# Kernel optimization log

Hardware: AMD Instinct MI355X
Metric: run time of the kernel (lower is better)

The kernel has to match this reference:

```python
import jax, jax.numpy as jnp
import numpy as np

DIM = 128
B, H, W = 2, 256, 256


def conv2d(x, w, b, groups=1):
    # x: [B,C,H,W], w: [O, C//groups, kh, kw] (OIHW)
    y = jax.lax.conv_general_dilated(
        x, w, window_strides=(1, 1), padding='SAME',
        dimension_numbers=('NCHW', 'OIHW', 'NCHW'),
        feature_group_count=groups)
    return y + b[None, :, None, None]


def l2_normalize(x, axis=-1, eps=1e-12):
    # matches torch.nn.functional.normalize (p=2)
    n = jnp.sqrt(jnp.sum(x * x, axis=axis, keepdims=True))
    return x / jnp.maximum(n, eps)


def setup_inputs() -> dict:
    key = jax.random.key(0)
    ks = jax.random.split(key, 14)
    d = DIM
    h = d // 2
    s = 0.05
    return {
        'x': jax.random.normal(ks[0], (B, d, H, W), dtype=jnp.float32),
        'w_qkv': jax.random.normal(ks[1], (3 * d, d, 1, 1), dtype=jnp.float32) * s,
        'b_qkv': jax.random.normal(ks[2], (3 * d,), dtype=jnp.float32) * s,
        'w_q': jax.random.normal(ks[3], (d, 1, 3, 3), dtype=jnp.float32) * s,
        'b_q': jax.random.normal(ks[4], (d,), dtype=jnp.float32) * s,
        'w_k': jax.random.normal(ks[5], (d, 1, 3, 3), dtype=jnp.float32) * s,
        'b_k': jax.random.normal(ks[6], (d,), dtype=jnp.float32) * s,
        'w_v1': jax.random.normal(ks[7], (h, 2, 3, 3), dtype=jnp.float32) * s,  # groups=d/2, 2 in-ch per group
        'b_v1': jax.random.normal(ks[8], (h,), dtype=jnp.float32) * s,
        'w_v2': jax.random.normal(ks[9], (h, 1, 3, 3), dtype=jnp.float32) * s,  # depthwise on d/2
        'b_v2': jax.random.normal(ks[10], (h,), dtype=jnp.float32) * s,
        'temperature': jnp.ones((d, 1, 1), dtype=jnp.float32),
        'w_po': jax.random.normal(ks[11], (d, d, 1, 1), dtype=jnp.float32) * s,
        'b_po': jax.random.normal(ks[12], (d,), dtype=jnp.float32) * s,
    }


def reference(x, w_qkv, b_qkv, w_q, b_q, w_k, b_k, w_v1, b_v1, w_v2, b_v2,
              temperature, w_po, b_po):
    d = x.shape[1]
    h = d // 2
    # 1x1 conv -> qkv, then split
    qkv = conv2d(x, w_qkv, b_qkv)                     # [B,3d,H,W]
    q, k, v = jnp.split(qkv, 3, axis=1)
    # depthwise 3x3 on q, k
    q = conv2d(q, w_q, b_q, groups=d)
    k = conv2d(k, w_k, b_k, groups=d)
    # MDC on v: grouped conv (2->1 per group), depthwise, concat, sigmoid gate
    x1 = conv2d(v, w_v1, b_v1, groups=h)              # [B,d/2,H,W]
    x2 = conv2d(x1, w_v2, b_v2, groups=h)             # [B,d/2,H,W]
    v = jax.nn.sigmoid(v) * jnp.concatenate([x1, x2], axis=1)
    # per-channel row attention: normalize over W, [B,C,H,H] scores
    q1 = l2_normalize(q, axis=-1)
    k1 = l2_normalize(k, axis=-1)
    scores = jnp.einsum('bchw,bcgw->bchg', q1, k1) * temperature[None]  # [B,C,H,H]
    attn = jax.nn.softmax(scores, axis=-1)
    out = jnp.einsum('bchg,bcgw->bchw', attn, v)      # [B,C,H,W]
    return conv2d(out, w_po, b_po)
```

## Files before the change

kernel.cpp:

```cpp
#include <hip/hip_runtime.h>

typedef unsigned short u16;
typedef unsigned int u32;

#define HW 256
#define PIX 65536

#define WS_T1   100663296ull
#define WS_K1   134217728ull
#define WS_VP   167772160ull
#define WS_NEED 201326592ull

typedef __attribute__((ext_vector_type(8))) short s8v;
typedef __attribute__((ext_vector_type(4))) float f4v;

__device__ __forceinline__ float bu2f(u16 u){ union{u32 i; float f;} x; x.i=((u32)u)<<16; return x.f; }
__device__ __forceinline__ u16 f2bu(float f){ union{float f; u32 i;} x; x.f=f; u32 i=x.i; return (u16)((i + 0x7FFFu + ((i>>16)&1u))>>16); }
__device__ __forceinline__ float sigm(float x){ return 1.0f/(1.0f+__expf(-x)); }
__device__ __forceinline__ u16 cvt_el(float v){ return f2bu(v); }
__device__ __forceinline__ u16 cvt_el(u16 v){ return v; }
__device__ __forceinline__ int swz(int r, int c){ return r*256 + (((c>>3) ^ (r&7))<<3) + (c&7); }
__device__ __forceinline__ int pswz(int p, int c){ return (p<<7) + (((c>>3) ^ (p&7))<<3) + (c&7); }
__device__ __forceinline__ int vt_el(int w, int gb){
  int q = (w & 15) ^ gb ^ ((w >> 4) & 7);
  return ((w >> 4) << 10) + (gb << 7) + (q << 3);
}

template<int OC, typename TIN, bool F32>
__global__ __launch_bounds__(256,1) void k_gemmP(const TIN* __restrict__ in, const float* __restrict__ Wg,
                                                 const float* __restrict__ bias, int O_total,
                                                 void* __restrict__ outv){
  extern __shared__ u16 lds[];
  u16* Wl = lds;
  u16* Xl = lds + OC*128;
  int t = threadIdx.x;
  for (int i = t; i < OC*128; i += 256){
    int o = i >> 7, c = i & 127;
    Wl[(o << 7) | (c ^ ((o & 7) << 3))] = f2bu(Wg[(size_t)o*128 + c]);
  }
  int p_blk = blockIdx.x * 256;
  int b = p_blk >> 16;
  int p0 = p_blk & 65535;
  {
    const TIN* col = in + (size_t)b*128*PIX + p0 + t;
    #pragma unroll 8
    for (int c2 = 0; c2 < 64; ++c2){
      int c = c2 * 2;
      u16 v0 = cvt_el(col[(size_t)c*PIX]);
      u16 v1 = cvt_el(col[(size_t)(c+1)*PIX]);
      *(u32*)(Xl + pswz(t, c)) = (u32)v0 | ((u32)v1 << 16);
    }
  }
  __syncthreads();

  int wv = t >> 6, l = t & 63;
  int lg = l >> 4, lr = l & 15;
  int p_in0 = p0 + wv*16 + lr;

  s8v bf[4][4];
  #pragma unroll
  for (int pt = 0; pt < 4; ++pt){
    int p = wv*16 + pt*64 + lr;
    #pragma unroll
    for (int ks = 0; ks < 4; ++ks)
      bf[pt][ks] = *(const s8v*)(Xl + pswz(p, ks*32 + lg*8));
  }

  for (int ot = 0; ot < OC / 16; ++ot){
    f4v acc[4];
    #pragma unroll
    for (int pt = 0; pt < 4; ++pt) acc[pt] = (f4v){0.f,0.f,0.f,0.f};
    int o = (ot << 4) + lr;
    const u16* wl = Wl + (o << 7);
    int sw = (o & 7) << 3;
    #pragma unroll
    for (int ks = 0; ks < 4; ++ks){
      s8v a = *(const s8v*)(wl + ((((ks << 5) + (lg << 3)) ^ sw)));
      #pragma unroll
      for (int pt = 0; pt < 4; ++pt)
        acc[pt] = __builtin_amdgcn_mfma_f32_16x16x32_bf16(a, bf[pt][ks], acc[pt], 0, 0, 0);
    }
    #pragma unroll
    for (int j = 0; j < 4; ++j){
      int o_row = (ot << 4) + (lg << 2) + j;
      float bv = bias[o_row];
      size_t base = ((size_t)(b * O_total + o_row)) << 16;
      #pragma unroll
      for (int pt = 0; pt < 4; ++pt){
        if (F32){
          ((float*)outv)[base + p_in0 + pt*64] = acc[pt][j] + bv;
        } else {
          ((u16*)outv)[base + p_in0 + pt*64] = f2bu(acc[pt][j] + bv);
        }
      }
    }
  }
}
#define GP384_LDS ((384*128 + 256*128) * 2)
#define GP128_LDS ((128*128 + 256*128) * 2)

__global__ __launch_bounds__(256) void k_dwqk2(const u16* __restrict__ qkv,
                                               const float* __restrict__ w_q, const float* __restrict__ b_q,
                                               const float* __restrict__ w_k, const float* __restrict__ b_k,
                                               u16* __restrict__ q1, u16* __restrict__ k1){
  __shared__ u16 ins[18*272];
  int t = threadIdx.x;
  int chunk = blockIdx.x;
  int c = blockIdx.y;
  int which = blockIdx.z & 1, b = blockIdx.z >> 1;
  const u16* in = qkv + ((size_t)(b*384 + which*128 + c)) * PIX;

  #pragma unroll
  for (int i = t; i < 612; i += 256) ((uint4*)ins)[i] = make_uint4(0,0,0,0);
  __syncthreads();
  int r0 = chunk*16 - 1;
  for (int i = t; i < 576; i += 256){
    int j = i >> 5, k = i & 31;
    int r = r0 + j;
    if (r >= 0 && r < HW)
      *(uint4*)(ins + j*272 + 8 + k*8) = *(const uint4*)(in + r*HW + k*8);
  }
  __syncthreads();

  const float* wk = (which ? w_k : w_q) + c*9;
  float K0=wk[0],K1=wk[1],K2=wk[2],K3=wk[3],K4=wk[4],K5=wk[5],K6=wk[6],K7=wk[7],K8=wk[8];
  float bias = (which ? b_k : b_q)[c];

  int wv = t >> 6, l = t & 63;
  int cb = l * 4;
  float wr[3][6];
  auto ldrow = [&](int j, int slot){
    ushort4 m = *(const ushort4*)(ins + j*272 + 8 + cb);
    wr[slot][0] = bu2f(ins[j*272 + 7 + cb]);
    wr[slot][1] = bu2f(m.x); wr[slot][2] = bu2f(m.y);
    wr[slot][3] = bu2f(m.z); wr[slot][4] = bu2f(m.w);
    wr[slot][5] = bu2f(ins[j*272 + 12 + cb]);
  };
  int rb = wv * 4;
  ldrow(rb, 0); ldrow(rb+1, 1);
  u16* outp = (which ? k1 : q1) + ((size_t)(b*128 + c)) * PIX;
  #pragma unroll
  for (int s = 0; s < 4; ++s){
    ldrow(rb + s + 2, (s+2)%3);
    const float* T = wr[s%3];
    const float* M = wr[(s+1)%3];
    const float* Bo = wr[(s+2)%3];
    float o[4]; float ss = 0.f;
    #pragma unroll
    for (int d = 0; d < 4; ++d){
      float a = bias;
      a = fmaf(K0, T[d], a);  a = fmaf(K1, T[d+1], a);  a = fmaf(K2, T[d+2], a);
      a = fmaf(K3, M[d], a);  a = fmaf(K4, M[d+1], a);  a = fmaf(K5, M[d+2], a);
      a = fmaf(K6, Bo[d], a); a = fmaf(K7, Bo[d+1], a); a = fmaf(K8, Bo[d+2], a);
      o[d] = a;
      ss = fmaf(a, a, ss);
    }
    #pragma unroll
    for (int m = 1; m < 64; m <<= 1) ss += __shfl_xor(ss, m, 64);
    float sc = 1.0f / fmaxf(sqrtf(ss), 1e-12f);
    int row = chunk*16 + rb + s;
    ushort4 pk;
    pk.x = f2bu(o[0]*sc); pk.y = f2bu(o[1]*sc); pk.z = f2bu(o[2]*sc); pk.w = f2bu(o[3]*sc);
    *(ushort4*)(outp + row*HW + cb) = pk;
  }
}

#define MDC_LDS (2*36*272*2 + 34*272*4)

__global__ __launch_bounds__(256,1) void k_mdc2(const u16* __restrict__ qkv,
                                                const float* __restrict__ w_v1, const float* __restrict__ b_v1,
                                                const float* __restrict__ w_v2, const float* __restrict__ b_v2,
                                                u16* __restrict__ vp){
  extern __shared__ char sm[];
  u16*   ins = (u16*)sm;
  float* x1s = (float*)(sm + 2*36*272*2);
  int t = threadIdx.x;
  int chunk = blockIdx.x;
  int g = blockIdx.y;
  int b = blockIdx.z;
  const u16* vbase = qkv + ((size_t)(b*384 + 256)) * PIX;

  #pragma unroll
  for (int i = t; i < 2*36*34; i += 256) ((uint4*)ins)[i] = make_uint4(0,0,0,0);
  for (int i = t; i < 34*68; i += 256) ((uint4*)x1s)[i] = make_uint4(0,0,0,0);
  __syncthreads();
  int r0 = chunk*32 - 2;
  #pragma unroll
  for (int ch = 0; ch < 2; ++ch){
    const u16* src = vbase + (size_t)(2*g + ch) * PIX;
    for (int i = t; i < 1152; i += 256){
      int j = i >> 5, k = i & 31;
      int r = r0 + j;
      if (r >= 0 && r < HW)
        *(uint4*)(ins + ch*36*272 + j*272 + 8 + k*8) = *(const uint4*)(src + r*HW + k*8);
    }
  }
  __syncthreads();

  float W1[18];
  #pragma unroll
  for (int i = 0; i < 18; ++i) W1[i] = w_v1[g*18 + i];
  float B1 = b_v1[g];
  int cb = t + 8;
  float win[2][3][3];
  #pragma unroll
  for (int ch = 0; ch < 2; ++ch)
    #pragma unroll
    for (int rr = 0; rr < 2; ++rr)
      #pragma unroll
      for (int k = 0; k < 3; ++k)
        win[ch][rr][k] = bu2f(ins[ch*36*272 + rr*272 + cb - 1 + k]);
  #pragma unroll
  for (int j = 0; j < 34; ++j){
    #pragma unroll
    for (int ch = 0; ch < 2; ++ch)
      #pragma unroll
      for (int k = 0; k < 3; ++k)
        win[ch][(j+2)%3][k] = bu2f(ins[ch*36*272 + (j+2)*272 + cb - 1 + k]);
    float v = B1;
    #pragma unroll
    for (int ch = 0; ch < 2; ++ch)
      #pragma unroll
      for (int i = 0; i < 3; ++i)
        #pragma unroll
        for (int k = 0; k < 3; ++k)
          v = fmaf(W1[ch*9 + i*3 + k], win[ch][(j+i)%3][k], v);
    int gr = chunk*32 - 1 + j;
    if (gr >= 0 && gr < HW) x1s[j*272 + cb] = v;
  }
  __syncthreads();

  float W2[9];
  #pragma unroll
  for (int i = 0; i < 9; ++i) W2[i] = w_v2[g*9 + i];
  float B2 = b_v2[g];
  const u16* vg   = vbase + (size_t)g * PIX;
  const u16* vg64 = vbase + (size_t)(64 + g) * PIX;
  u16* out0 = vp + ((size_t)(b*128 + g)) * PIX;
  u16* out1 = vp + ((size_t)(b*128 + 64 + g)) * PIX;
  float xw[3][3];
  #pragma unroll
  for (int rr = 0; rr < 2; ++rr)
    #pragma unroll
    for (int k = 0; k < 3; ++k)
      xw[rr][k] = x1s[rr*272 + cb - 1 + k];
  #pragma unroll
  for (int h = 0; h < 32; ++h){
    #pragma unroll
    for (int k = 0; k < 3; ++k)
      xw[(h+2)%3][k] = x1s[(h+2)*272 + cb - 1 + k];
    float x2 = B2;
    #pragma unroll
    for (int i = 0; i < 3; ++i)
      #pragma unroll
      for (int k = 0; k < 3; ++k)
        x2 = fmaf(W2[i*3 + k], xw[(h+i)%3][k], x2);
    int gr = chunk*32 + h;
    float g1 = sigm(bu2f(vg[gr*HW + t]));
    float g2 = sigm(bu2f(vg64[gr*HW + t]));
    float x1c = xw[(h+1)%3][1];
    out0[gr*HW + t] = f2bu(g1 * x1c);
    out1[gr*HW + t] = f2bu(g2 * x2);
  }
}

#define AT2_LDS 163840

__global__ __launch_bounds__(512,1) void k_attn2(const u16* __restrict__ q1, const u16* __restrict__ k1,
                                                 const u16* __restrict__ vp, const float* __restrict__ temp,
                                                 u16* __restrict__ out){
  extern __shared__ char smemraw[];
  u16* Qs = (u16*)smemraw;
  u16* Ks = Qs + 32768;
  u16* Ps = Ks + 16384;
  const int t = threadIdx.x;
  const int l = t & 63;
  const int wv = t >> 6;
  const int c15 = l & 15, h = l >> 4;
  const int blk = blockIdx.x;
  const int plane = blk >> 1, hf = blk & 1;
  const u16* qp  = q1 + (size_t)plane * PIX + hf*128*HW;
  const u16* kp  = k1 + (size_t)plane * PIX;
  const u16* vpp = vp + (size_t)plane * PIX;
  u16* op = out + (size_t)plane * PIX + hf*128*HW;
  const float tc = temp[plane & 127];

  #pragma unroll
  for (int i = 0; i < 8; ++i){
    int c = t + i*512; int row = c >> 5, bc = (c & 31) << 3;
    *(uint4*)(Qs + swz(row, bc)) = *(const uint4*)(qp + row*HW + bc);
  }
  #pragma unroll
  for (int i = 0; i < 4; ++i){
    int c = t + i*512; int row = c >> 5, bc = (c & 31) << 3;
    *(uint4*)(Ks + swz(row, bc)) = *(const uint4*)(kp + row*HW + bc);
  }
  __syncthreads();

  const int r_a = wv*16 + c15;
  s8v qa[8];
  #pragma unroll
  for (int ks = 0; ks < 8; ++ks)
    qa[ks] = *(const s8v*)(Qs + swz(r_a, ks*32 + h*8));

  f4v sacc[16];
  #pragma unroll
  for (int i = 0; i < 16; ++i) sacc[i] = (f4v){0.f,0.f,0.f,0.f};

  uint4 pf[4];
  #pragma unroll
  for (int gt = 0; gt < 4; ++gt){
    {
      const u16* src = (gt < 3) ? (kp + (gt+1)*64*HW) : vpp;
      #pragma unroll
      for (int i = 0; i < 4; ++i){
        int c = t + i*512; int row = c >> 5, bc = (c & 31) << 3;
        pf[i] = *(const uint4*)(src + row*HW + bc);
      }
    }
    #pragma unroll
    for (int gi = 0; gi < 4; ++gi){
      f4v acc = sacc[gt*4 + gi];
      #pragma unroll
      for (int ks = 0; ks < 8; ++ks){
        s8v b = *(const s8v*)(Ks + swz(gi*16 + c15, ks*32 + h*8));
        acc = __builtin_amdgcn_mfma_f32_16x16x32_bf16(qa[ks], b, acc, 0, 0, 0);
      }
      sacc[gt*4 + gi] = acc;
    }
    __syncthreads();
    #pragma unroll
    for (int i = 0; i < 4; ++i){
      int c = t + i*512; int row = c >> 5, bc = (c & 31) << 3;
      *(uint4*)(Ks + swz(row, bc)) = pf[i];
    }
    __syncthreads();
  }

  float mj[4] = {-1e30f,-1e30f,-1e30f,-1e30f};
  #pragma unroll
  for (int i = 0; i < 16; ++i)
    #pragma unroll
    for (int j = 0; j < 4; ++j){
      sacc[i][j] *= tc;
      mj[j] = fmaxf(mj[j], sacc[i][j]);
    }
  #pragma unroll
  for (int j = 0; j < 4; ++j){
    mj[j] = fmaxf(mj[j], __shfl_xor(mj[j], 1, 64));
    mj[j] = fmaxf(mj[j], __shfl_xor(mj[j], 2, 64));
    mj[j] = fmaxf(mj[j], __shfl_xor(mj[j], 4, 64));
    mj[j] = fmaxf(mj[j], __shfl_xor(mj[j], 8, 64));
  }
  float sj[4] = {0.f,0.f,0.f,0.f};
  #pragma unroll
  for (int i = 0; i < 16; ++i)
    #pragma unroll
    for (int j = 0; j < 4; ++j){
      float e = __expf(sacc[i][j] - mj[j]);
      sacc[i][j] = e;
      sj[j] += e;
    }
  #pragma unroll
  for (int j = 0; j < 4; ++j){
    sj[j] += __shfl_xor(sj[j], 1, 64);
    sj[j] += __shfl_xor(sj[j], 2, 64);
    sj[j] += __shfl_xor(sj[j], 4, 64);
    sj[j] += __shfl_xor(sj[j], 8, 64);
    sj[j] = 1.0f / sj[j];
  }
  #pragma unroll
  for (int i = 0; i < 16; ++i)
    #pragma unroll
    for (int j = 0; j < 4; ++j)
      Ps[swz(wv*16 + h*4 + j, i*16 + c15)] = f2bu(sacc[i][j] * sj[j]);
  __syncthreads();

  f4v oacc[16];
  #pragma unroll
  for (int i = 0; i < 16; ++i) oacc[i] = (f4v){0.f,0.f,0.f,0.f};

  #pragma unroll
  for (int gt = 0; gt < 4; ++gt){
    if (gt < 3){
      #pragma unroll
      for (int i = 0; i < 4; ++i){
        int c = t + i*512; int row = c >> 5, bc = (c & 31) << 3;
        pf[i] = *(const uint4*)(vpp + (gt+1)*64*HW + row*HW + bc);
      }
    }
    if (t < 256){
      int gb = t >> 5, wb = t & 31;
      u32 rr[8][4];
      #pragma unroll
      for (int i = 0; i < 8; ++i){
        uint4 v = *(const uint4*)(Ks + (gb*8 + i)*256 + ((wb ^ i) << 3));
        rr[i][0] = v.x; rr[i][1] = v.y; rr[i][2] = v.z; rr[i][3] = v.w;
      }
      #pragma unroll
      for (int j = 0; j < 8; ++j){
        u32 sel = (j & 1) ? 0x07060302u : 0x05040100u;
        int jh = j >> 1;
        u32 o0 = __builtin_amdgcn_perm(rr[1][jh], rr[0][jh], sel);
        u32 o1 = __builtin_amdgcn_perm(rr[3][jh], rr[2][jh], sel);
        u32 o2 = __builtin_amdgcn_perm(rr[5][jh], rr[4][jh], sel);
        u32 o3 = __builtin_amdgcn_perm(rr[7][jh], rr[6][jh], sel);
        int w = wb*8 + j;
        *(uint4*)(Qs + vt_el(w, gb)) = make_uint4(o0, o1, o2, o3);
      }
    }
    __syncthreads();
    if (gt < 3){
      #pragma unroll
      for (int i = 0; i < 4; ++i){
        int c = t + i*512; int row = c >> 5, bc = (c & 31) << 3;
        *(uint4*)(Ks + swz(row, bc)) = pf[i];
      }
    }
    s8v pa[2];
    #pragma unroll
    for (int k2 = 0; k2 < 2; ++k2)
      pa[k2] = *(const s8v*)(Ps + swz(r_a, gt*64 + k2*32 + h*8));
    #pragma unroll
    for (int wt = 0; wt < 16; ++wt){
      f4v acc = oacc[wt];
      #pragma unroll
      for (int k2 = 0; k2 < 2; ++k2){
        int w = wt*16 + c15;
        s8v b = *(const s8v*)(Qs + vt_el(w, (k2 << 2) + h));
        acc = __builtin_amdgcn_mfma_f32_16x16x32_bf16(pa[k2], b, acc, 0, 0, 0);
      }
      oacc[wt] = acc;
    }
    __syncthreads();
  }

  #pragma unroll
  for (int wt = 0; wt < 16; ++wt)
    #pragma unroll
    for (int j = 0; j < 4; ++j)
      Qs[swz(wv*16 + h*4 + j, wt*16 + c15)] = f2bu(oacc[wt][j]);
  __syncthreads();
  #pragma unroll
  for (int i = 0; i < 8; ++i){
    int row = wv*16 + i*2 + (l >> 5);
    int bc = (l & 31) << 3;
    uint4 v = *(const uint4*)(Qs + swz(row, bc));
    *(uint4*)(op + row*HW + bc) = v;
  }
}

extern "C" void kernel_launch(void* const* d_in, const int* in_sizes, int n_in,
                              void* d_out, int out_size, void* d_ws, size_t ws_size,
                              hipStream_t stream){
  (void)in_sizes; (void)n_in; (void)out_size;
  if (ws_size < (size_t)WS_NEED) return;

  const float* x     = (const float*)d_in[0];
  const float* w_qkv = (const float*)d_in[1];
  const float* b_qkv = (const float*)d_in[2];
  const float* w_q   = (const float*)d_in[3];
  const float* b_q   = (const float*)d_in[4];
  const float* w_k   = (const float*)d_in[5];
  const float* b_k   = (const float*)d_in[6];
  const float* w_v1  = (const float*)d_in[7];
  const float* b_v1  = (const float*)d_in[8];
  const float* w_v2  = (const float*)d_in[9];
  const float* b_v2  = (const float*)d_in[10];
  const float* temp  = (const float*)d_in[11];
  const float* w_po  = (const float*)d_in[12];
  const float* b_po  = (const float*)d_in[13];

  char* ws = (char*)d_ws;
  u16*  qkv = (u16*)ws;
  u16*  q1  = (u16*)(ws + WS_T1);
  u16*  k1  = (u16*)(ws + WS_K1);
  u16*  vp  = (u16*)(ws + WS_VP);
  u16*  aout = qkv;
  float* out = (float*)d_out;

  (void)hipFuncSetAttribute((const void*)k_gemmP<384, float, false>, hipFuncAttributeMaxDynamicSharedMemorySize, GP384_LDS);
  (void)hipFuncSetAttribute((const void*)k_gemmP<128, u16, true>,   hipFuncAttributeMaxDynamicSharedMemorySize, GP128_LDS);

  k_gemmP<384, float, false><<<512, 256, GP384_LDS, stream>>>(x, w_qkv, b_qkv, 384, (void*)qkv);
  k_dwqk2<<<dim3(16, 128, 4), 256, 0, stream>>>(qkv, w_q, b_q, w_k, b_k, q1, k1);
  (void)hipFuncSetAttribute((const void*)k_mdc2, hipFuncAttributeMaxDynamicSharedMemorySize, MDC_LDS);
  k_mdc2<<<dim3(8, 64, 2), 256, MDC_LDS, stream>>>(qkv, w_v1, b_v1, w_v2, b_v2, vp);
  (void)hipFuncSetAttribute((const void*)k_attn2, hipFuncAttributeMaxDynamicSharedMemorySize, AT2_LDS);
  k_attn2<<<512, 512, AT2_LDS, stream>>>(q1, k1, vp, temp, aout);
  k_gemmP<128, u16, true><<<512, 256, GP128_LDS, stream>>>(aout, w_po, b_po, 128, (void*)out);
}
```

Baseline: 257.2 us.

## Double GEMM block threads and vectorize LDS staging of input tiles

The 1x1-conv GEMM kernels now run with 512 threads per block instead of 256. Each wave covers 32 pixels instead of 64, which halves the per-wave accumulator and fragment registers. The input tile is staged with 16-byte LDS stores, and the bf16 path reads two pixels per 32-bit global load. This aims to add latency hiding and cut the number of load and store instructions in the staging phase. The cost is more waves per block sharing one LDS tile, and each weight fragment load now feeds fewer MFMAs.

```diff
diff --git a/kernel.cpp b/kernel.cpp
--- a/kernel.cpp
+++ b/kernel.cpp
@@ -27,58 +27,78 @@
 }
 
 template<int OC, typename TIN, bool F32>
-__global__ __launch_bounds__(256,1) void k_gemmP(const TIN* __restrict__ in, const float* __restrict__ Wg,
-                                                 const float* __restrict__ bias, int O_total,
-                                                 void* __restrict__ outv){
+__global__ __launch_bounds__(512,1) void k_gemmP2(const TIN* __restrict__ in, const float* __restrict__ Wg,
+                                                  const float* __restrict__ bias, int O_total,
+                                                  void* __restrict__ outv){
   extern __shared__ u16 lds[];
   u16* Wl = lds;
   u16* Xl = lds + OC*128;
   int t = threadIdx.x;
-  for (int i = t; i < OC*128; i += 256){
+  for (int i = t; i < OC*128; i += 512){
     int o = i >> 7, c = i & 127;
     Wl[(o << 7) | (c ^ ((o & 7) << 3))] = f2bu(Wg[(size_t)o*128 + c]);
   }
   int p_blk = blockIdx.x * 256;
   int b = p_blk >> 16;
   int p0 = p_blk & 65535;
-  {
-    const TIN* col = in + (size_t)b*128*PIX + p0 + t;
-    #pragma unroll 8
-    for (int c2 = 0; c2 < 64; ++c2){
-      int c = c2 * 2;
-      u16 v0 = cvt_el(col[(size_t)c*PIX]);
-      u16 v1 = cvt_el(col[(size_t)(c+1)*PIX]);
-      *(u32*)(Xl + pswz(t, c)) = (u32)v0 | ((u32)v1 << 16);
+  if (sizeof(TIN) == 4){
+    int p = t & 255, half = (t >> 8) * 64;
+    const float* col = (const float*)in + ((size_t)(b*128 + half))*PIX + p0 + p;
+    #pragma unroll
+    for (int c8 = 0; c8 < 8; ++c8){
+      u32 pk[4];
+      #pragma unroll
+      for (int j = 0; j < 4; ++j){
+        u16 v0 = f2bu(col[(size_t)(c8*8 + 2*j)*PIX]);
+        u16 v1 = f2bu(col[(size_t)(c8*8 + 2*j + 1)*PIX]);
+        pk[j] = (u32)v0 | ((u32)v1 << 16);
+      }
+      *(uint4*)(Xl + pswz(p, half + c8*8)) = make_uint4(pk[0],pk[1],pk[2],pk[3]);
+    }
+  } else {
+    int p = (t & 127) * 2, quarter = (t >> 7) * 32;
+    const u16* col = (const u16*)in + ((size_t)(b*128 + quarter))*PIX + p0 + p;
+    #pragma unroll
+    for (int c8 = 0; c8 < 4; ++c8){
+      u32 va[4], vb[4];
+      #pragma unroll
+      for (int j = 0; j < 4; ++j){
+        u32 w0 = *(const u32*)(col + (size_t)(c8*8 + 2*j)*PIX);
+        u32 w1 = *(const u32*)(col + (size_t)(c8*8 + 2*j + 1)*PIX);
+        va[j] = (w0 & 0xFFFFu) | (w1 << 16);
+        vb[j] = (w0 >> 16) | (w1 & 0xFFFF0000u);
+      }
+      *(uint4*)(Xl + pswz(p,     quarter + c8*8)) = make_uint4(va[0],va[1],va[2],va[3]);
+      *(uint4*)(Xl + pswz(p + 1, quarter + c8*8)) = make_uint4(vb[0],vb[1],vb[2],vb[3]);
     }
   }
   __syncthreads();
 
   int wv = t >> 6, l = t & 63;
   int lg = l >> 4, lr = l & 15;
-  int p_in0 = p0 + wv*16 + lr;
-
-  s8v bf[4][4];
-  #pragma unroll
-  for (int pt = 0; pt < 4; ++pt){
-    int p = wv*16 + pt*64 + lr;
+  int p_in0 = p0 + wv*32 + lr;
+
+  s8v bf[2][4];
+  #pragma unroll
+  for (int pt = 0; pt < 2; ++pt){
+    int p = wv*32 + pt*16 + lr;
     #pragma unroll
     for (int ks = 0; ks < 4; ++ks)
       bf[pt][ks] = *(const s8v*)(Xl + pswz(p, ks*32 + lg*8));
   }
 
   for (int ot = 0; ot < OC / 16; ++ot){
-    f4v acc[4];
-    #pragma unroll
-    for (int pt = 0; pt < 4; ++pt) acc[pt] = (f4v){0.f,0.f,0.f,0.f};
+    f4v acc[2];
+    acc[0] = (f4v){0.f,0.f,0.f,0.f};
+    acc[1] = (f4v){0.f,0.f,0.f,0.f};
     int o = (ot << 4) + lr;
     const u16* wl = Wl + (o << 7);
     int sw = (o & 7) << 3;
     #pragma unroll
     for (int ks = 0; ks < 4; ++ks){
       s8v a = *(const s8v*)(wl + ((((ks << 5) + (lg << 3)) ^ sw)));
-      #pragma unroll
-      for (int pt = 0; pt < 4; ++pt)
-        acc[pt] = __builtin_amdgcn_mfma_f32_16x16x32_bf16(a, bf[pt][ks], acc[pt], 0, 0, 0);
+      acc[0] = __builtin_amdgcn_mfma_f32_16x16x32_bf16(a, bf[0][ks], acc[0], 0, 0, 0);
+      acc[1] = __builtin_amdgcn_mfma_f32_16x16x32_bf16(a, bf[1][ks], acc[1], 0, 0, 0);
     }
     #pragma unroll
     for (int j = 0; j < 4; ++j){
@@ -86,11 +106,11 @@
       float bv = bias[o_row];
       size_t base = ((size_t)(b * O_total + o_row)) << 16;
       #pragma unroll
-      for (int pt = 0; pt < 4; ++pt){
+      for (int pt = 0; pt < 2; ++pt){
         if (F32){
-          ((float*)outv)[base + p_in0 + pt*64] = acc[pt][j] + bv;
+          ((float*)outv)[base + p_in0 + pt*16] = acc[pt][j] + bv;
         } else {
-          ((u16*)outv)[base + p_in0 + pt*64] = f2bu(acc[pt][j] + bv);
+          ((u16*)outv)[base + p_in0 + pt*16] = f2bu(acc[pt][j] + bv);
         }
       }
     }
@@ -479,14 +499,14 @@
   u16*  aout = qkv;
   float* out = (float*)d_out;
 
-  (void)hipFuncSetAttribute((const void*)k_gemmP<384, float, false>, hipFuncAttributeMaxDynamicSharedMemorySize, GP384_LDS);
-  (void)hipFuncSetAttribute((const void*)k_gemmP<128, u16, true>,   hipFuncAttributeMaxDynamicSharedMemorySize, GP128_LDS);
-
-  k_gemmP<384, float, false><<<512, 256, GP384_LDS, stream>>>(x, w_qkv, b_qkv, 384, (void*)qkv);
+  (void)hipFuncSetAttribute((const void*)k_gemmP2<384, float, false>, hipFuncAttributeMaxDynamicSharedMemorySize, GP384_LDS);
+  (void)hipFuncSetAttribute((const void*)k_gemmP2<128, u16, true>,   hipFuncAttributeMaxDynamicSharedMemorySize, GP128_LDS);
+
+  k_gemmP2<384, float, false><<<512, 512, GP384_LDS, stream>>>(x, w_qkv, b_qkv, 384, (void*)qkv);
   k_dwqk2<<<dim3(16, 128, 4), 256, 0, stream>>>(qkv, w_q, b_q, w_k, b_k, q1, k1);
   (void)hipFuncSetAttribute((const void*)k_mdc2, hipFuncAttributeMaxDynamicSharedMemorySize, MDC_LDS);
   k_mdc2<<<dim3(8, 64, 2), 256, MDC_LDS, stream>>>(qkv, w_v1, b_v1, w_v2, b_v2, vp);
   (void)hipFuncSetAttribute((const void*)k_attn2, hipFuncAttributeMaxDynamicSharedMemorySize, AT2_LDS);
   k_attn2<<<512, 512, AT2_LDS, stream>>>(q1, k1, vp, temp, aout);
-  k_gemmP<128, u16, true><<<512, 256, GP128_LDS, stream>>>(aout, w_po, b_po, 128, (void*)out);
+  k_gemmP2<128, u16, true><<<512, 512, GP128_LDS, stream>>>(aout, w_po, b_po, 128, (void*)out);
 }
```

Result: faster. 235.6 us (-8.4%).
